# Kernel tuning notes

Hardware: AMD Instinct MI355X
Metric: run time of the kernel (lower is better)

## Reference

```python
import jax, jax.numpy as jnp
import numpy as np

L, D, H, KV, HD, KVL, I, PL = 8, 2048, 8, 2, 256, 4096, 8192, 256
FULL = (4,)          # layers with full (global) attention / global RoPE
POS = 2047           # current decode position (cache write slot)
N_REP = H // KV      # GQA expansion factor


def rms(x, eps=1e-6):
    # RMSNorm without scale (v_norm); scale applied by caller where needed
    return x * jax.lax.rsqrt(jnp.mean(x * x, axis=-1, keepdims=True) + eps)


def rope(x, cos, sin):
    half = HD // 2
    rot = jnp.concatenate([-x[..., half:], x[..., :half]], axis=-1)
    return x * cos + rot * sin


def _rope_tables(theta):
    inv = 1.0 / (theta ** (np.arange(0, HD, 2, dtype=np.float32) / HD))
    ang = jnp.asarray(POS * inv, dtype=jnp.float32)
    return jnp.concatenate([jnp.cos(ang)] * 2), jnp.concatenate([jnp.sin(ang)] * 2)


def setup_inputs() -> dict:
    key = jax.random.key(0)
    ks = jax.random.split(key, 24)
    r = lambda k, s, sc=0.02: jax.random.normal(k, s, jnp.float32) * sc
    gains = lambda k, s: 1.0 + jax.random.normal(k, s, jnp.float32) * 0.02
    cos_s, sin_s = _rope_tables(10000.0)
    cos_f, sin_f = _rope_tables(1000000.0)
    um = jnp.zeros((1, 1, KVL, 1), jnp.float32).at[0, 0, POS, 0].set(1.0)
    mask = jnp.where(jnp.arange(KVL) <= POS, 0.0, -1e9).astype(jnp.float32)
    return {
        "hidden_states": r(ks[0], (1, 1, D), 1.0),
        "causal_mask": mask,
        "update_mask": um,
        "per_layer_combined": r(ks[1], (1, 1, L * PL), 1.0),
        "cos_s": cos_s, "sin_s": sin_s, "cos_f": cos_f, "sin_f": sin_f,
        "K_in": r(ks[2], (L, KV, KVL, HD)),
        "V_in": r(ks[3], (L, KV, KVL, HD)),
        "w_q": r(ks[4], (L, H * HD, D)),
        "w_k": r(ks[5], (L, KV * HD, D)),
        "w_v": r(ks[6], (L, KV * HD, D)),
        "w_o": r(ks[7], (L, D, H * HD)),
        "g_in_ln": gains(ks[8], (L, D)),
        "g_q_norm": gains(ks[9], (L, HD)),
        "g_k_norm": gains(ks[10], (L, HD)),
        "g_post_attn_ln": gains(ks[11], (L, D)),
        "g_pre_ff_ln": gains(ks[12], (L, D)),
        "g_post_ff_ln": gains(ks[13], (L, D)),
        "w_gate": r(ks[14], (L, I, D)),
        "w_up": r(ks[15], (L, I, D)),
        "w_down": r(ks[16], (L, D, I)),
        "w_plg": r(ks[17], (L, PL, D)),
        "w_plp": r(ks[18], (L, D, PL)),
        "g_post_pl_ln": gains(ks[19], (L, D)),
        "layer_scalar": jnp.ones((L,), jnp.float32),
    }


def reference(hidden_states, causal_mask, update_mask, per_layer_combined,
              cos_s, sin_s, cos_f, sin_f, K_in, V_in,
              w_q, w_k, w_v, w_o,
              g_in_ln, g_q_norm, g_k_norm, g_post_attn_ln, g_pre_ff_ln, g_post_ff_ln,
              w_gate, w_up, w_down, w_plg, w_plp, g_post_pl_ln, layer_scalar):
    um = update_mask[0, 0]          # [KVL,1] one-hot at write position
    h = hidden_states[0, 0]         # [D], batch=1/seq=1 decode
    K_outs, V_outs = [], []
    for i in range(L):
        cos, sin = (cos_f, sin_f) if i in FULL else (cos_s, sin_s)
        # --- attention block ---
        res = h
        x = rms(h) * g_in_ln[i]
        q = rms((w_q[i] @ x).reshape(H, HD)) * g_q_norm[i]
        q = rope(q, cos, sin)                                   # [H,HD]
        k = rms((w_k[i] @ x).reshape(KV, HD)) * g_k_norm[i]
        k = rope(k, cos, sin)                                   # [KV,HD]
        v = rms((w_v[i] @ x).reshape(KV, HD))                    # v_norm (no scale)
        # full-tensor masked blend = KV cache write (faithful to source)
        Ko = K_in[i] * (1.0 - um) + k[:, None, :] * um          # [KV,KVL,HD]
        Vo = V_in[i] * (1.0 - um) + v[:, None, :] * um
        K_outs.append(Ko); V_outs.append(Vo)
        Ke = jnp.repeat(Ko, N_REP, axis=0)                      # GQA expand [H,KVL,HD]
        Ve = jnp.repeat(Vo, N_REP, axis=0)
        scores = jnp.einsum('hd,hkd->hk', q, Ke) + causal_mask  # no 1/sqrt(hd) in source
        attn = jax.nn.softmax(scores, axis=-1)
        ao = jnp.einsum('hk,hkd->hd', attn, Ve).reshape(H * HD)
        ao = rms(w_o[i] @ ao) * g_post_attn_ln[i]
        h = res + ao
        # --- gated MLP ---
        res = h
        xm = rms(h) * g_pre_ff_ln[i]
        m = w_down[i] @ (jax.nn.gelu(w_gate[i] @ xm, approximate=True) * (w_up[i] @ xm))
        h = res + rms(m) * g_post_ff_ln[i]
        # --- per-layer input gating ---
        res = h
        pls = per_layer_combined[0, 0, i * PL:(i + 1) * PL]     # [PL]
        g = jax.nn.gelu(w_plg[i] @ h, approximate=True) * pls
        h = res + rms(w_plp[i] @ g) * g_post_pl_ln[i]
        h = h * layer_scalar[i]
    return (h[None, None, :], jnp.stack(K_outs), jnp.stack(V_outs))
```

## Files before the change

kernel.cpp:

```cpp
#include <hip/hip_runtime.h>

#define NL   8
#define DIM  2048
#define NH   8
#define NKV  2
#define HD   256
#define KVL  4096
#define FFI  8192
#define PLD  256
#define POS  2047
#define NCH  128
#define CP   16

typedef float vfloat4 __attribute__((ext_vector_type(4)));

__device__ __forceinline__ float dot4(float4 a, float4 b){
  return a.x*b.x + a.y*b.y + a.z*b.z + a.w*b.w;
}

__device__ __forceinline__ float4 ntld4(const float4* p){
  vfloat4 v = __builtin_nontemporal_load((const vfloat4*)p);
  float4 r; r.x=v.x; r.y=v.y; r.z=v.z; r.w=v.w; return r;
}
__device__ __forceinline__ void ntst4(float4* p, float4 v){
  vfloat4 t; t.x=v.x; t.y=v.y; t.z=v.z; t.w=v.w;
  __builtin_nontemporal_store(t, (vfloat4*)p);
}

__device__ __forceinline__ float waveAllSum(float v){
#pragma unroll
  for(int o=1;o<64;o<<=1) v += __shfl_xor(v,o,64);
  return v;
}

__device__ __forceinline__ float blockSum256(float v, float* red){
  int lane = threadIdx.x & 63, w = threadIdx.x >> 6;
  v = waveAllSum(v);
  __syncthreads();
  if(lane==0) red[w] = v;
  __syncthreads();
  return red[0]+red[1]+red[2]+red[3];
}

__device__ __forceinline__ float gelu_tanh(float v){
  return 0.5f*v*(1.0f + tanhf(0.7978845608028654f*(v + 0.044715f*v*v*v)));
}

__device__ __forceinline__ float4 normRope(const float* __restrict__ raw, int lane,
    const float* __restrict__ gain, const float* __restrict__ cosT,
    const float* __restrict__ sinT, bool doRope){
  float4 v4 = ((const float4*)raw)[lane];
  float ss = waveAllSum(dot4(v4,v4));
  float sc = rsqrtf(ss*(1.f/HD) + 1e-6f);
  float4 n;
  if(gain){
    float4 g4 = ((const float4*)gain)[lane];
    n.x=v4.x*sc*g4.x; n.y=v4.y*sc*g4.y; n.z=v4.z*sc*g4.z; n.w=v4.w*sc*g4.w;
  } else {
    n.x=v4.x*sc; n.y=v4.y*sc; n.z=v4.z*sc; n.w=v4.w*sc;
  }
  if(!doRope) return n;
  float4 np;
  np.x=__shfl_xor(n.x,32,64); np.y=__shfl_xor(n.y,32,64);
  np.z=__shfl_xor(n.z,32,64); np.w=__shfl_xor(n.w,32,64);
  float4 c4 = ((const float4*)cosT)[lane];
  float4 s4 = ((const float4*)sinT)[lane];
  float sg = (lane < 32) ? -1.f : 1.f;
  float4 o;
  o.x = n.x*c4.x + sg*np.x*s4.x;
  o.y = n.y*c4.y + sg*np.y*s4.y;
  o.z = n.z*c4.z + sg*np.z*s4.z;
  o.w = n.w*c4.w + sg*np.w*s4.w;
  return o;
}

__global__ __launch_bounds__(256) void qkv_k(
    const float* __restrict__ Wq, const float* __restrict__ Wk,
    const float* __restrict__ Wv,
    const float* __restrict__ hFF, const float* __restrict__ u,
    const float* __restrict__ g_pl, const float* __restrict__ lsc,
    const float* __restrict__ g_in, const float* __restrict__ hidden,
    float* __restrict__ hRes, float* __restrict__ qkv){
  __shared__ float xs[DIM];
  __shared__ float red[4];
  int tid = threadIdx.x;
  float hv[8];
  if(hidden){
#pragma unroll
    for(int i=0;i<8;i++) hv[i] = hidden[tid + i*256];
  } else {
    float uv[8]; float ss1 = 0.f;
#pragma unroll
    for(int i=0;i<8;i++){ uv[i] = u[tid + i*256]; ss1 += uv[i]*uv[i]; }
    ss1 = blockSum256(ss1, red);
    float r1 = rsqrtf(ss1*(1.f/DIM) + 1e-6f);
    float ls = lsc[0];
#pragma unroll
    for(int i=0;i<8;i++){
      int idx = tid + i*256;
      hv[i] = (hFF[idx] + uv[i]*r1*g_pl[idx])*ls;
    }
  }
  float ss2 = 0.f;
#pragma unroll
  for(int i=0;i<8;i++) ss2 += hv[i]*hv[i];
  ss2 = blockSum256(ss2, red);
  float r2 = rsqrtf(ss2*(1.f/DIM) + 1e-6f);
#pragma unroll
  for(int i=0;i<8;i++){
    int idx = tid + i*256;
    xs[idx] = hv[i]*r2*g_in[idx];
    if(blockIdx.x==0) hRes[idx] = hv[i];
  }
  __syncthreads();
  int lane = tid & 63, wv = tid >> 6;
  int r = blockIdx.x*4 + wv;
  const float* W; int row;
  if(r < 2048){ W = Wq; row = r; }
  else if(r < 2560){ W = Wk; row = r - 2048; }
  else { W = Wv; row = r - 2560; }
  const float4* Wr = (const float4*)(W + (size_t)row*DIM);
  const float4* xs4 = (const float4*)xs;
  float4 w8[8];
#pragma unroll
  for(int i=0;i<8;i++) w8[i] = Wr[i*64+lane];
  float acc = 0.f;
#pragma unroll
  for(int i=0;i<8;i++) acc += dot4(w8[i], xs4[i*64+lane]);
  acc = waveAllSum(acc);
  if(lane==0) qkv[r] = acc;
}

__global__ __launch_bounds__(256) void attn_k(
    const float* __restrict__ qkvb,
    const float* __restrict__ gq, const float* __restrict__ gk,
    const float* __restrict__ cosT, const float* __restrict__ sinT,
    const float* __restrict__ Ki, const float* __restrict__ Vi,
    float* __restrict__ Kl, float* __restrict__ Vl,
    float* __restrict__ pm, float* __restrict__ pl, float* __restrict__ po){
  int b = blockIdx.x, tid = threadIdx.x, lane = tid & 63, wv = tid >> 6;

  if(b == NKV*NCH){
    int kvv = wv >> 1, isV = wv & 1;
    const float* raw = qkvb + (isV ? 2560 : 2048) + kvv*HD;
    float4 o = normRope(raw, lane, isV ? nullptr : gk, cosT, sinT, !isV);
    float* dst = (isV ? Vl : Kl) + ((size_t)kvv*KVL + POS)*HD;
    ((float4*)dst)[lane] = o;
    return;
  }
  if(b > NKV*NCH){
    int b2 = b - (NKV*NCH+1);
#pragma unroll
    for(int i=0;i<8;i++){
      int ri = b2*32 + wv*8 + i;
      int combo = ri >> 11;
      int pos = 2048 + (ri & 2047);
      size_t off = ((size_t)(combo&1)*KVL + pos)*HD;
      const float4* s = (const float4*)(((combo>>1) ? Vi : Ki) + off);
      float4* d = (float4*)(((combo>>1) ? Vl : Kl) + off);
      ntst4(d + lane, ntld4(s + lane));
    }
    return;
  }

  int kv = b & 1, c = b >> 1;
  __shared__ float q_s[4][HD];
  __shared__ float vf_s[HD];
  __shared__ float s_s[4][CP];
  __shared__ float s_w[4][CP];
  bool fresh = (c == NCH-1);

  { float4 o = normRope(qkvb + (kv*4 + wv)*HD, lane, gq, cosT, sinT, true);
    ((float4*)q_s[wv])[lane] = o; }
  float4 kf4 = {0,0,0,0};
  if(fresh){
    if(wv == 3) kf4 = normRope(qkvb + 2048 + kv*HD, lane, gk, cosT, sinT, true);
    if(wv == 1){
      float4 o = normRope(qkvb + 2560 + kv*HD, lane, nullptr, cosT, sinT, false);
      ((float4*)vf_s)[lane] = o;
    }
  }
  __syncthreads();

  float4 q4[4];
#pragma unroll
  for(int hh=0;hh<4;hh++) q4[hh] = ((const float4*)q_s[hh])[lane];
  const float4* Kp = (const float4*)(Ki + ((size_t)kv*KVL + c*CP)*HD);
  float4* Kd = (float4*)(Kl + ((size_t)kv*KVL + c*CP)*HD);
#pragma unroll
  for(int j=0;j<4;j++){
    int p = wv*4 + j;
    bool isFreshRow = (fresh && p==CP-1);
    float4 k4;
    if(isFreshRow) k4 = kf4;
    else {
      k4 = Kp[(size_t)p*64 + lane];
      ntst4(Kd + (size_t)p*64 + lane, k4);
    }
    float d0 = dot4(k4,q4[0]), d1 = dot4(k4,q4[1]);
    float d2 = dot4(k4,q4[2]), d3 = dot4(k4,q4[3]);
    d0 = waveAllSum(d0); d1 = waveAllSum(d1);
    d2 = waveAllSum(d2); d3 = waveAllSum(d3);
    if(lane==0){ s_s[0][p]=d0; s_s[1][p]=d1; s_s[2][p]=d2; s_s[3][p]=d3; }
  }
  __syncthreads();

  if(tid < 64){
    int hh = tid >> 4, pp = tid & 15;
    float s = s_s[hh][pp];
    float m = s;
#pragma unroll
    for(int o=1;o<16;o<<=1) m = fmaxf(m, __shfl_xor(m,o,64));
    float e = __expf(s - m);
    float ls = e;
#pragma unroll
    for(int o=1;o<16;o<<=1) ls += __shfl_xor(ls,o,64);
    s_w[hh][pp] = e;
    if(pp==0){ int hg = kv*4 + hh; pm[hg*NCH + c] = m; pl[hg*NCH + c] = ls; }
  }
  __syncthreads();

  int d = tid;
  const float* Vp = Vi + ((size_t)kv*KVL + c*CP)*HD;
  float* Vd = Vl + ((size_t)kv*KVL + c*CP)*HD;
  float vv[CP];
#pragma unroll
  for(int p2=0;p2<CP;p2++){
    bool isFreshRow = (fresh && p2==CP-1);
    if(isFreshRow) vv[p2] = vf_s[d];
    else {
      vv[p2] = Vp[(size_t)p2*HD + d];
      Vd[(size_t)p2*HD + d] = vv[p2];
    }
  }
  float acc[4] = {0.f,0.f,0.f,0.f};
#pragma unroll
  for(int p2=0;p2<CP;p2++){
#pragma unroll
    for(int hh=0;hh<4;hh++) acc[hh] += s_w[hh][p2]*vv[p2];
  }
#pragma unroll
  for(int hh=0;hh<4;hh++)
    po[((size_t)(kv*4+hh)*NCH + c)*HD + d] = acc[hh];
}

__global__ __launch_bounds__(256) void attn_c(const float* __restrict__ pm,
    const float* __restrict__ pl, const float* __restrict__ po, float* __restrict__ ao){
  int h = blockIdx.x, tid = threadIdx.x;
  __shared__ float sm[NCH], sl[NCH], se[NCH];
  if(tid < NCH){ sm[tid] = pm[h*NCH+tid]; sl[tid] = pl[h*NCH+tid]; }
  __syncthreads();
  float M = -1e30f;
  for(int c=0;c<NCH;c++) M = fmaxf(M, sm[c]);
  if(tid < NCH) se[tid] = __expf(sm[tid]-M);
  __syncthreads();
  float Lh = 0.f;
  for(int c=0;c<NCH;c++) Lh += sl[c]*se[c];
  float a0=0.f, a1=0.f, a2=0.f, a3=0.f;
#pragma unroll 1
  for(int c=0;c<NCH;c+=4){
    a0 += po[((size_t)h*NCH + c  )*HD + tid]*se[c];
    a1 += po[((size_t)h*NCH + c+1)*HD + tid]*se[c+1];
    a2 += po[((size_t)h*NCH + c+2)*HD + tid]*se[c+2];
    a3 += po[((size_t)h*NCH + c+3)*HD + tid]*se[c+3];
  }
  ao[h*HD + tid] = (a0+a1+a2+a3) / Lh;
}

template<int C>
__global__ __launch_bounds__(256) void gemv_k(const float* __restrict__ W,
    const float* __restrict__ x, float* __restrict__ y){
  __shared__ float xs[C];
  for(int i=threadIdx.x; i<C/4; i+=256)
    ((float4*)xs)[i] = ((const float4*)x)[i];
  __syncthreads();
  int lane = threadIdx.x & 63, wv = threadIdx.x >> 6;
  int r = blockIdx.x*4 + wv;
  const float4* Wr = (const float4*)(W + (size_t)r*C);
  const float4* xs4 = (const float4*)xs;
  float acc = 0.f;
#pragma unroll
  for(int ii=0;ii<C/2048;ii++){
    float4 w8[8];
#pragma unroll
    for(int i=0;i<8 && ii*8+i < C/256;i++) w8[i] = Wr[(ii*8+i)*64+lane];
#pragma unroll
    for(int i=0;i<8 && ii*8+i < C/256;i++) acc += dot4(w8[i], xs4[(ii*8+i)*64+lane]);
  }
  if(C < 2048){
    float4 w1 = Wr[lane];
    acc = dot4(w1, xs4[lane]);
  }
  acc = waveAllSum(acc);
  if(lane==0) y[r] = acc;
}

__global__ __launch_bounds__(256) void gateup_k(const float* __restrict__ Wg,
    const float* __restrict__ Wu, const float* __restrict__ y,
    const float* __restrict__ hRes, const float* __restrict__ g_pa,
    const float* __restrict__ g_pf, float* __restrict__ hMid, float* __restrict__ t){
  __shared__ float xs[DIM];
  __shared__ float red[4];
  int tid = threadIdx.x;
  float yv[8]; float ss1 = 0.f;
#pragma unroll
  for(int i=0;i<8;i++){ yv[i] = y[tid + i*256]; ss1 += yv[i]*yv[i]; }
  ss1 = blockSum256(ss1, red);
  float r1 = rsqrtf(ss1*(1.f/DIM) + 1e-6f);
  float hv[8]; float ss2 = 0.f;
#pragma unroll
  for(int i=0;i<8;i++){
    int idx = tid + i*256;
    hv[i] = hRes[idx] + yv[i]*r1*g_pa[idx];
    ss2 += hv[i]*hv[i];
  }
  ss2 = blockSum256(ss2, red);
  float r2 = rsqrtf(ss2*(1.f/DIM) + 1e-6f);
#pragma unroll
  for(int i=0;i<8;i++){
    int idx = tid + i*256;
    xs[idx] = hv[i]*r2*g_pf[idx];
    if(blockIdx.x==0) hMid[idx] = hv[i];
  }
  __syncthreads();
  int lane = tid & 63, wv = tid >> 6;
  int j = blockIdx.x*4 + wv;
  const float4* Gr = (const float4*)(Wg + (size_t)j*DIM);
  const float4* Ur = (const float4*)(Wu + (size_t)j*DIM);
  const float4* xs4 = (const float4*)xs;
  float4 g8[8], u8[8];
#pragma unroll
  for(int i=0;i<8;i++) g8[i] = Gr[i*64+lane];
#pragma unroll
  for(int i=0;i<8;i++) u8[i] = Ur[i*64+lane];
  float ag = 0.f, au = 0.f;
#pragma unroll
  for(int i=0;i<8;i++){
    float4 bv = xs4[i*64+lane];
    ag += dot4(g8[i], bv);
    au += dot4(u8[i], bv);
  }
  ag = waveAllSum(ag);
  au = waveAllSum(au);
  if(lane==0) t[j] = gelu_tanh(ag)*au;
}

__global__ __launch_bounds__(256) void down_k(const float* __restrict__ Wd,
    const float* __restrict__ t, float* __restrict__ mv){
  __shared__ float red[4];
  int tid = threadIdx.x, lane = tid & 63, wv = tid >> 6;
  int r = blockIdx.x;
  const float4* Wr = (const float4*)(Wd + (size_t)r*FFI) + wv*512;
  const float4* tp = (const float4*)t + wv*512;
  float4 w8[8], t8[8];
#pragma unroll
  for(int i=0;i<8;i++) w8[i] = Wr[i*64+lane];
#pragma unroll
  for(int i=0;i<8;i++) t8[i] = tp[i*64+lane];
  float acc = 0.f;
#pragma unroll
  for(int i=0;i<8;i++) acc += dot4(w8[i], t8[i]);
  acc = waveAllSum(acc);
  if(lane==0) red[wv] = acc;
  __syncthreads();
  if(tid==0) mv[r] = red[0]+red[1]+red[2]+red[3];
}

__global__ __launch_bounds__(256) void plg_k(const float* __restrict__ W,
    const float* __restrict__ mv, const float* __restrict__ hMid,
    const float* __restrict__ g_ff, const float* __restrict__ pls,
    float* __restrict__ hFFout, float* __restrict__ gb){
  __shared__ float xs[DIM];
  __shared__ float red[4];
  int tid = threadIdx.x;
  float mvv[8]; float ss1 = 0.f;
#pragma unroll
  for(int i=0;i<8;i++){ mvv[i] = mv[tid + i*256]; ss1 += mvv[i]*mvv[i]; }
  ss1 = blockSum256(ss1, red);
  float r1 = rsqrtf(ss1*(1.f/DIM) + 1e-6f);
#pragma unroll
  for(int i=0;i<8;i++){
    int idx = tid + i*256;
    float hc = hMid[idx] + mvv[i]*r1*g_ff[idx];
    xs[idx] = hc;
    if(blockIdx.x==0) hFFout[idx] = hc;
  }
  __syncthreads();
  int lane = tid & 63, wv = tid >> 6;
  int r = blockIdx.x*4 + wv;
  const float4* Wr = (const float4*)(W + (size_t)r*DIM);
  const float4* xs4 = (const float4*)xs;
  float4 w8[8];
#pragma unroll
  for(int i=0;i<8;i++) w8[i] = Wr[i*64+lane];
  float acc = 0.f;
#pragma unroll
  for(int i=0;i<8;i++) acc += dot4(w8[i], xs4[i*64+lane]);
  acc = waveAllSum(acc);
  if(lane==0) gb[r] = gelu_tanh(acc)*pls[r];
}

__global__ __launch_bounds__(256) void final_k(const float* __restrict__ u,
    const float* __restrict__ hFF, const float* __restrict__ g_pl,
    const float* __restrict__ lsc, float* __restrict__ out){
  __shared__ float red[4];
  int tid = threadIdx.x;
  float uv[8]; float ss1 = 0.f;
#pragma unroll
  for(int i=0;i<8;i++){ uv[i] = u[tid + i*256]; ss1 += uv[i]*uv[i]; }
  ss1 = blockSum256(ss1, red);
  float r1 = rsqrtf(ss1*(1.f/DIM) + 1e-6f);
  float ls = lsc[0];
#pragma unroll
  for(int i=0;i<8;i++){
    int idx = tid + i*256;
    out[idx] = (hFF[idx] + uv[i]*r1*g_pl[idx])*ls;
  }
}

extern "C" void kernel_launch(void* const* d_in, const int* in_sizes, int n_in,
                              void* d_out, int out_size, void* d_ws, size_t ws_size,
                              hipStream_t stream){
  const float* hidden   = (const float*)d_in[0];
  const float* plc      = (const float*)d_in[3];
  const float* cos_s    = (const float*)d_in[4];
  const float* sin_s    = (const float*)d_in[5];
  const float* cos_f    = (const float*)d_in[6];
  const float* sin_f    = (const float*)d_in[7];
  const float* K_in     = (const float*)d_in[8];
  const float* V_in     = (const float*)d_in[9];
  const float* w_q      = (const float*)d_in[10];
  const float* w_k      = (const float*)d_in[11];
  const float* w_v      = (const float*)d_in[12];
  const float* w_o      = (const float*)d_in[13];
  const float* g_in_ln  = (const float*)d_in[14];
  const float* g_q_norm = (const float*)d_in[15];
  const float* g_k_norm = (const float*)d_in[16];
  const float* g_pa_ln  = (const float*)d_in[17];
  const float* g_pf_ln  = (const float*)d_in[18];
  const float* g_ff_ln  = (const float*)d_in[19];
  const float* w_gate   = (const float*)d_in[20];
  const float* w_up     = (const float*)d_in[21];
  const float* w_down   = (const float*)d_in[22];
  const float* w_plg    = (const float*)d_in[23];
  const float* w_plp    = (const float*)d_in[24];
  const float* g_pl_ln  = (const float*)d_in[25];
  const float* l_scal   = (const float*)d_in[26];

  float* out  = (float*)d_out;
  float* outK = out + DIM;
  float* outV = outK + (size_t)NL*NKV*KVL*HD;

  float* ws   = (float*)d_ws;
  float* hRes = ws;
  float* hMid = ws + 2048;
  float* hFF  = ws + 4096;
  float* qkvb = ws + 6144;
  float* y    = ws + 9216;
  float* t    = ws + 11264;
  float* mv   = ws + 19456;
  float* gb   = ws + 21504;
  float* u    = ws + 21760;
  float* pm   = ws + 23808;
  float* pl   = ws + 24832;
  float* po   = ws + 25856;
  float* ao   = ws + 288000;

  for(int l=0;l<NL;l++){
    const float* cosT = (l==4) ? cos_f : cos_s;
    const float* sinT = (l==4) ? sin_f : sin_s;
    float* Kl = outK + (size_t)l*NKV*KVL*HD;
    float* Vl = outV + (size_t)l*NKV*KVL*HD;
    const float* Ki = K_in + (size_t)l*NKV*KVL*HD;
    const float* Vi = V_in + (size_t)l*NKV*KVL*HD;

    qkv_k<<<768,256,0,stream>>>(
        w_q + (size_t)l*NH*HD*DIM, w_k + (size_t)l*NKV*HD*DIM,
        w_v + (size_t)l*NKV*HD*DIM,
        hFF, u,
        (l>0) ? g_pl_ln + (size_t)(l-1)*DIM : g_pl_ln,
        (l>0) ? l_scal + (l-1) : l_scal,
        g_in_ln + (size_t)l*DIM,
        (l==0) ? hidden : nullptr,
        hRes, qkvb);

    attn_k<<<NKV*NCH+1+256,256,0,stream>>>(qkvb, g_q_norm + l*HD,
                                           g_k_norm + l*HD, cosT, sinT,
                                           Ki, Vi, Kl, Vl, pm, pl, po);

    attn_c<<<NH,256,0,stream>>>(pm, pl, po, ao);

    gemv_k<DIM><<<512,256,0,stream>>>(w_o + (size_t)l*DIM*NH*HD, ao, y);

    gateup_k<<<FFI/4,256,0,stream>>>(w_gate + (size_t)l*FFI*DIM,
                                     w_up + (size_t)l*FFI*DIM,
                                     y, hRes, g_pa_ln + (size_t)l*DIM,
                                     g_pf_ln + (size_t)l*DIM, hMid, t);

    down_k<<<DIM,256,0,stream>>>(w_down + (size_t)l*DIM*FFI, t, mv);

    plg_k<<<PLD/4,256,0,stream>>>(w_plg + (size_t)l*PLD*DIM, mv, hMid,
                                  g_ff_ln + (size_t)l*DIM, plc + l*PLD, hFF, gb);

    gemv_k<PLD><<<512,256,0,stream>>>(w_plp + (size_t)l*DIM*PLD, gb, u);
  }

  final_k<<<1,256,0,stream>>>(u, hFF, g_pl_ln + (size_t)(NL-1)*DIM,
                              l_scal + (NL-1), out);
}
```

Before: 787.8 us.

## Fuse dependent attention and FFN-tail stages into single kernels via atomic counters

Merges attention, attention-combine and o-projection into one launch, and down-proj, per-layer gate, per-layer projection and final norm into another. Later-stage blocks spin on global atomic counters until producer blocks signal completion. The goal is to cut kernel launch gaps and tail bubbles between the many small dependent stages. It depends on producer blocks being scheduled before consumers, which is not guaranteed and could deadlock, and it adds a memset plus spin-wait overhead.

```diff
diff --git a/kernel.cpp b/kernel.cpp
--- a/kernel.cpp
+++ b/kernel.cpp
@@ -74,6 +74,22 @@
   return o;
 }
 
+__device__ __forceinline__ void prodSignal(unsigned* c){
+  __syncthreads();
+  if(threadIdx.x == 0){
+    __builtin_amdgcn_fence(__ATOMIC_RELEASE, "agent");
+    __hip_atomic_fetch_add(c, 1u, __ATOMIC_RELAXED, __HIP_MEMORY_SCOPE_AGENT);
+  }
+}
+__device__ __forceinline__ void consWait(unsigned* c, unsigned n){
+  if(threadIdx.x == 0){
+    while(__hip_atomic_load(c, __ATOMIC_RELAXED, __HIP_MEMORY_SCOPE_AGENT) < n)
+      __builtin_amdgcn_s_sleep(2);
+    __builtin_amdgcn_fence(__ATOMIC_ACQUIRE, "agent");
+  }
+  __syncthreads();
+}
+
 __global__ __launch_bounds__(256) void qkv_k(
     const float* __restrict__ Wq, const float* __restrict__ Wk,
     const float* __restrict__ Wv,
@@ -131,25 +147,105 @@
   if(lane==0) qkv[r] = acc;
 }
 
-__global__ __launch_bounds__(256) void attn_k(
+__global__ __launch_bounds__(256,5) void attnfull_k(
     const float* __restrict__ qkvb,
     const float* __restrict__ gq, const float* __restrict__ gk,
     const float* __restrict__ cosT, const float* __restrict__ sinT,
     const float* __restrict__ Ki, const float* __restrict__ Vi,
     float* __restrict__ Kl, float* __restrict__ Vl,
-    float* __restrict__ pm, float* __restrict__ pl, float* __restrict__ po){
+    float* __restrict__ pm, float* __restrict__ pl, float* __restrict__ po,
+    const float* __restrict__ Wo, float* __restrict__ ao, float* __restrict__ y,
+    unsigned* cnt){
+  __shared__ float sh[2048];
   int b = blockIdx.x, tid = threadIdx.x, lane = tid & 63, wv = tid >> 6;
-
-  if(b == NKV*NCH){
+  unsigned* c_attn = cnt;
+  unsigned* c_comb = cnt + 16;
+
+  if(b < NKV*NCH){
+    int kv = b & 1, c = b >> 1;
+    float* q_s  = sh;
+    float* vf_s = sh + 1024;
+    float* s_sB = sh + 1280;
+    float* s_wB = sh + 1344;
+    bool fresh = (c == NCH-1);
+    { float4 o = normRope(qkvb + (kv*4 + wv)*HD, lane, gq, cosT, sinT, true);
+      ((float4*)(q_s + wv*HD))[lane] = o; }
+    float4 kf4 = {0,0,0,0};
+    if(fresh){
+      if(wv == 3) kf4 = normRope(qkvb + 2048 + kv*HD, lane, gk, cosT, sinT, true);
+      if(wv == 1){
+        float4 o = normRope(qkvb + 2560 + kv*HD, lane, nullptr, cosT, sinT, false);
+        ((float4*)vf_s)[lane] = o;
+      }
+    }
+    __syncthreads();
+    float4 q4[4];
+#pragma unroll
+    for(int hh=0;hh<4;hh++) q4[hh] = ((const float4*)(q_s + hh*HD))[lane];
+    const float4* Kp = (const float4*)(Ki + ((size_t)kv*KVL + c*CP)*HD);
+    float4* Kd = (float4*)(Kl + ((size_t)kv*KVL + c*CP)*HD);
+#pragma unroll
+    for(int j=0;j<4;j++){
+      int p = wv*4 + j;
+      bool isFreshRow = (fresh && p==CP-1);
+      float4 k4;
+      if(isFreshRow) k4 = kf4;
+      else {
+        k4 = Kp[(size_t)p*64 + lane];
+        ntst4(Kd + (size_t)p*64 + lane, k4);
+      }
+      float d0 = dot4(k4,q4[0]), d1 = dot4(k4,q4[1]);
+      float d2 = dot4(k4,q4[2]), d3 = dot4(k4,q4[3]);
+      d0 = waveAllSum(d0); d1 = waveAllSum(d1);
+      d2 = waveAllSum(d2); d3 = waveAllSum(d3);
+      if(lane==0){ s_sB[0*CP+p]=d0; s_sB[1*CP+p]=d1; s_sB[2*CP+p]=d2; s_sB[3*CP+p]=d3; }
+    }
+    __syncthreads();
+    if(tid < 64){
+      int hh = tid >> 4, pp = tid & 15;
+      float s = s_sB[hh*CP+pp];
+      float m = s;
+#pragma unroll
+      for(int o=1;o<16;o<<=1) m = fmaxf(m, __shfl_xor(m,o,64));
+      float e = __expf(s - m);
+      float ls = e;
+#pragma unroll
+      for(int o=1;o<16;o<<=1) ls += __shfl_xor(ls,o,64);
+      s_wB[hh*CP+pp] = e;
+      if(pp==0){ int hg = kv*4 + hh; pm[hg*NCH + c] = m; pl[hg*NCH + c] = ls; }
+    }
+    __syncthreads();
+    int d = tid;
+    const float* Vp = Vi + ((size_t)kv*KVL + c*CP)*HD;
+    float* Vd = Vl + ((size_t)kv*KVL + c*CP)*HD;
+    float vv[CP];
+#pragma unroll
+    for(int p2=0;p2<CP;p2++){
+      bool isFreshRow = (fresh && p2==CP-1);
+      if(isFreshRow) vv[p2] = vf_s[d];
+      else {
+        vv[p2] = Vp[(size_t)p2*HD + d];
+        Vd[(size_t)p2*HD + d] = vv[p2];
+      }
+    }
+    float acc[4] = {0.f,0.f,0.f,0.f};
+#pragma unroll
+    for(int p2=0;p2<CP;p2++){
+#pragma unroll
+      for(int hh=0;hh<4;hh++) acc[hh] += s_wB[hh*CP+p2]*vv[p2];
+    }
+#pragma unroll
+    for(int hh=0;hh<4;hh++)
+      po[((size_t)(kv*4+hh)*NCH + c)*HD + d] = acc[hh];
+    prodSignal(c_attn);
+  } else if(b == NKV*NCH){
     int kvv = wv >> 1, isV = wv & 1;
     const float* raw = qkvb + (isV ? 2560 : 2048) + kvv*HD;
     float4 o = normRope(raw, lane, isV ? nullptr : gk, cosT, sinT, !isV);
     float* dst = (isV ? Vl : Kl) + ((size_t)kvv*KVL + POS)*HD;
     ((float4*)dst)[lane] = o;
-    return;
-  }
-  if(b > NKV*NCH){
-    int b2 = b - (NKV*NCH+1);
+  } else if(b < 513){
+    int b2 = b - 257;
 #pragma unroll
     for(int i=0;i<8;i++){
       int ri = b2*32 + wv*8 + i;
@@ -160,139 +256,46 @@
       float4* d = (float4*)(((combo>>1) ? Vl : Kl) + off);
       ntst4(d + lane, ntld4(s + lane));
     }
-    return;
-  }
-
-  int kv = b & 1, c = b >> 1;
-  __shared__ float q_s[4][HD];
-  __shared__ float vf_s[HD];
-  __shared__ float s_s[4][CP];
-  __shared__ float s_w[4][CP];
-  bool fresh = (c == NCH-1);
-
-  { float4 o = normRope(qkvb + (kv*4 + wv)*HD, lane, gq, cosT, sinT, true);
-    ((float4*)q_s[wv])[lane] = o; }
-  float4 kf4 = {0,0,0,0};
-  if(fresh){
-    if(wv == 3) kf4 = normRope(qkvb + 2048 + kv*HD, lane, gk, cosT, sinT, true);
-    if(wv == 1){
-      float4 o = normRope(qkvb + 2560 + kv*HD, lane, nullptr, cosT, sinT, false);
-      ((float4*)vf_s)[lane] = o;
-    }
-  }
-  __syncthreads();
-
-  float4 q4[4];
-#pragma unroll
-  for(int hh=0;hh<4;hh++) q4[hh] = ((const float4*)q_s[hh])[lane];
-  const float4* Kp = (const float4*)(Ki + ((size_t)kv*KVL + c*CP)*HD);
-  float4* Kd = (float4*)(Kl + ((size_t)kv*KVL + c*CP)*HD);
-#pragma unroll
-  for(int j=0;j<4;j++){
-    int p = wv*4 + j;
-    bool isFreshRow = (fresh && p==CP-1);
-    float4 k4;
-    if(isFreshRow) k4 = kf4;
-    else {
-      k4 = Kp[(size_t)p*64 + lane];
-      ntst4(Kd + (size_t)p*64 + lane, k4);
-    }
-    float d0 = dot4(k4,q4[0]), d1 = dot4(k4,q4[1]);
-    float d2 = dot4(k4,q4[2]), d3 = dot4(k4,q4[3]);
-    d0 = waveAllSum(d0); d1 = waveAllSum(d1);
-    d2 = waveAllSum(d2); d3 = waveAllSum(d3);
-    if(lane==0){ s_s[0][p]=d0; s_s[1][p]=d1; s_s[2][p]=d2; s_s[3][p]=d3; }
-  }
-  __syncthreads();
-
-  if(tid < 64){
-    int hh = tid >> 4, pp = tid & 15;
-    float s = s_s[hh][pp];
-    float m = s;
-#pragma unroll
-    for(int o=1;o<16;o<<=1) m = fmaxf(m, __shfl_xor(m,o,64));
-    float e = __expf(s - m);
-    float ls = e;
-#pragma unroll
-    for(int o=1;o<16;o<<=1) ls += __shfl_xor(ls,o,64);
-    s_w[hh][pp] = e;
-    if(pp==0){ int hg = kv*4 + hh; pm[hg*NCH + c] = m; pl[hg*NCH + c] = ls; }
-  }
-  __syncthreads();
-
-  int d = tid;
-  const float* Vp = Vi + ((size_t)kv*KVL + c*CP)*HD;
-  float* Vd = Vl + ((size_t)kv*KVL + c*CP)*HD;
-  float vv[CP];
-#pragma unroll
-  for(int p2=0;p2<CP;p2++){
-    bool isFreshRow = (fresh && p2==CP-1);
-    if(isFreshRow) vv[p2] = vf_s[d];
-    else {
-      vv[p2] = Vp[(size_t)p2*HD + d];
-      Vd[(size_t)p2*HD + d] = vv[p2];
-    }
-  }
-  float acc[4] = {0.f,0.f,0.f,0.f};
-#pragma unroll
-  for(int p2=0;p2<CP;p2++){
-#pragma unroll
-    for(int hh=0;hh<4;hh++) acc[hh] += s_w[hh][p2]*vv[p2];
-  }
-#pragma unroll
-  for(int hh=0;hh<4;hh++)
-    po[((size_t)(kv*4+hh)*NCH + c)*HD + d] = acc[hh];
-}
-
-__global__ __launch_bounds__(256) void attn_c(const float* __restrict__ pm,
-    const float* __restrict__ pl, const float* __restrict__ po, float* __restrict__ ao){
-  int h = blockIdx.x, tid = threadIdx.x;
-  __shared__ float sm[NCH], sl[NCH], se[NCH];
-  if(tid < NCH){ sm[tid] = pm[h*NCH+tid]; sl[tid] = pl[h*NCH+tid]; }
-  __syncthreads();
-  float M = -1e30f;
-  for(int c=0;c<NCH;c++) M = fmaxf(M, sm[c]);
-  if(tid < NCH) se[tid] = __expf(sm[tid]-M);
-  __syncthreads();
-  float Lh = 0.f;
-  for(int c=0;c<NCH;c++) Lh += sl[c]*se[c];
-  float a0=0.f, a1=0.f, a2=0.f, a3=0.f;
+  } else if(b < 521){
+    consWait(c_attn, 256);
+    int h = b - 513;
+    float* sm = sh; float* sl = sh + 128; float* se = sh + 256;
+    if(tid < NCH){ sm[tid] = pm[h*NCH+tid]; sl[tid] = pl[h*NCH+tid]; }
+    __syncthreads();
+    float M = -1e30f;
+    for(int c=0;c<NCH;c++) M = fmaxf(M, sm[c]);
+    if(tid < NCH) se[tid] = __expf(sm[tid]-M);
+    __syncthreads();
+    float Lh = 0.f;
+    for(int c=0;c<NCH;c++) Lh += sl[c]*se[c];
+    float a0=0.f, a1=0.f, a2=0.f, a3=0.f;
 #pragma unroll 1
-  for(int c=0;c<NCH;c+=4){
-    a0 += po[((size_t)h*NCH + c  )*HD + tid]*se[c];
-    a1 += po[((size_t)h*NCH + c+1)*HD + tid]*se[c+1];
-    a2 += po[((size_t)h*NCH + c+2)*HD + tid]*se[c+2];
-    a3 += po[((size_t)h*NCH + c+3)*HD + tid]*se[c+3];
-  }
-  ao[h*HD + tid] = (a0+a1+a2+a3) / Lh;
-}
-
-template<int C>
-__global__ __launch_bounds__(256) void gemv_k(const float* __restrict__ W,
-    const float* __restrict__ x, float* __restrict__ y){
-  __shared__ float xs[C];
-  for(int i=threadIdx.x; i<C/4; i+=256)
-    ((float4*)xs)[i] = ((const float4*)x)[i];
-  __syncthreads();
-  int lane = threadIdx.x & 63, wv = threadIdx.x >> 6;
-  int r = blockIdx.x*4 + wv;
-  const float4* Wr = (const float4*)(W + (size_t)r*C);
-  const float4* xs4 = (const float4*)xs;
-  float acc = 0.f;
-#pragma unroll
-  for(int ii=0;ii<C/2048;ii++){
+    for(int c=0;c<NCH;c+=4){
+      a0 += po[((size_t)h*NCH + c  )*HD + tid]*se[c];
+      a1 += po[((size_t)h*NCH + c+1)*HD + tid]*se[c+1];
+      a2 += po[((size_t)h*NCH + c+2)*HD + tid]*se[c+2];
+      a3 += po[((size_t)h*NCH + c+3)*HD + tid]*se[c+3];
+    }
+    ao[h*HD + tid] = (a0+a1+a2+a3) / Lh;
+    prodSignal(c_comb);
+  } else {
+    consWait(c_comb, 8);
+    float4* sh4 = (float4*)sh;
+#pragma unroll
+    for(int i=0;i<2;i++) sh4[tid + i*256] = ((const float4*)ao)[tid + i*256];
+    __syncthreads();
+    int b2 = b - 521;
+    int r = b2*4 + wv;
+    const float4* Wr = (const float4*)(Wo + (size_t)r*DIM);
     float4 w8[8];
 #pragma unroll
-    for(int i=0;i<8 && ii*8+i < C/256;i++) w8[i] = Wr[(ii*8+i)*64+lane];
-#pragma unroll
-    for(int i=0;i<8 && ii*8+i < C/256;i++) acc += dot4(w8[i], xs4[(ii*8+i)*64+lane]);
-  }
-  if(C < 2048){
-    float4 w1 = Wr[lane];
-    acc = dot4(w1, xs4[lane]);
-  }
-  acc = waveAllSum(acc);
-  if(lane==0) y[r] = acc;
+    for(int i=0;i<8;i++) w8[i] = Wr[i*64+lane];
+    float acc = 0.f;
+#pragma unroll
+    for(int i=0;i<8;i++) acc += dot4(w8[i], sh4[i*64+lane]);
+    acc = waveAllSum(acc);
+    if(lane==0) y[r] = acc;
+  }
 }
 
 __global__ __launch_bounds__(256) void gateup_k(const float* __restrict__ Wg,
@@ -345,76 +348,101 @@
   if(lane==0) t[j] = gelu_tanh(ag)*au;
 }
 
-__global__ __launch_bounds__(256) void down_k(const float* __restrict__ Wd,
-    const float* __restrict__ t, float* __restrict__ mv){
-  __shared__ float red[4];
-  int tid = threadIdx.x, lane = tid & 63, wv = tid >> 6;
-  int r = blockIdx.x;
-  const float4* Wr = (const float4*)(Wd + (size_t)r*FFI) + wv*512;
-  const float4* tp = (const float4*)t + wv*512;
-  float4 w8[8], t8[8];
-#pragma unroll
-  for(int i=0;i<8;i++) w8[i] = Wr[i*64+lane];
-#pragma unroll
-  for(int i=0;i<8;i++) t8[i] = tp[i*64+lane];
-  float acc = 0.f;
-#pragma unroll
-  for(int i=0;i<8;i++) acc += dot4(w8[i], t8[i]);
-  acc = waveAllSum(acc);
-  if(lane==0) red[wv] = acc;
-  __syncthreads();
-  if(tid==0) mv[r] = red[0]+red[1]+red[2]+red[3];
-}
-
-__global__ __launch_bounds__(256) void plg_k(const float* __restrict__ W,
-    const float* __restrict__ mv, const float* __restrict__ hMid,
-    const float* __restrict__ g_ff, const float* __restrict__ pls,
-    float* __restrict__ hFFout, float* __restrict__ gb){
-  __shared__ float xs[DIM];
-  __shared__ float red[4];
-  int tid = threadIdx.x;
-  float mvv[8]; float ss1 = 0.f;
-#pragma unroll
-  for(int i=0;i<8;i++){ mvv[i] = mv[tid + i*256]; ss1 += mvv[i]*mvv[i]; }
-  ss1 = blockSum256(ss1, red);
-  float r1 = rsqrtf(ss1*(1.f/DIM) + 1e-6f);
-#pragma unroll
-  for(int i=0;i<8;i++){
-    int idx = tid + i*256;
-    float hc = hMid[idx] + mvv[i]*r1*g_ff[idx];
-    xs[idx] = hc;
-    if(blockIdx.x==0) hFFout[idx] = hc;
-  }
-  __syncthreads();
-  int lane = tid & 63, wv = tid >> 6;
-  int r = blockIdx.x*4 + wv;
-  const float4* Wr = (const float4*)(W + (size_t)r*DIM);
-  const float4* xs4 = (const float4*)xs;
-  float4 w8[8];
-#pragma unroll
-  for(int i=0;i<8;i++) w8[i] = Wr[i*64+lane];
-  float acc = 0.f;
-#pragma unroll
-  for(int i=0;i<8;i++) acc += dot4(w8[i], xs4[i*64+lane]);
-  acc = waveAllSum(acc);
-  if(lane==0) gb[r] = gelu_tanh(acc)*pls[r];
-}
-
-__global__ __launch_bounds__(256) void final_k(const float* __restrict__ u,
-    const float* __restrict__ hFF, const float* __restrict__ g_pl,
-    const float* __restrict__ lsc, float* __restrict__ out){
-  __shared__ float red[4];
-  int tid = threadIdx.x;
-  float uv[8]; float ss1 = 0.f;
-#pragma unroll
-  for(int i=0;i<8;i++){ uv[i] = u[tid + i*256]; ss1 += uv[i]*uv[i]; }
-  ss1 = blockSum256(ss1, red);
-  float r1 = rsqrtf(ss1*(1.f/DIM) + 1e-6f);
-  float ls = lsc[0];
-#pragma unroll
-  for(int i=0;i<8;i++){
-    int idx = tid + i*256;
-    out[idx] = (hFF[idx] + uv[i]*r1*g_pl[idx])*ls;
+__global__ __launch_bounds__(256,5) void downfull_k(
+    const float* __restrict__ Wd, const float* __restrict__ t,
+    float* __restrict__ mv,
+    const float* __restrict__ Wpg, const float* __restrict__ Wpp,
+    const float* __restrict__ hMid, const float* __restrict__ gff,
+    const float* __restrict__ pls, float* __restrict__ hFF,
+    float* __restrict__ gb, float* __restrict__ u,
+    const float* __restrict__ gpl, const float* __restrict__ lsc,
+    float* __restrict__ outv,
+    unsigned* cnt){
+  __shared__ float sh[2056];
+  int b = blockIdx.x, tid = threadIdx.x, lane = tid & 63, wv = tid >> 6;
+  unsigned* c_down = cnt + 32;
+  unsigned* c_plg  = cnt + 48;
+  unsigned* c_plp  = cnt + 64;
+
+  if(b < 1024){
+    int r0 = b*2;
+    int r = r0 + (wv>>1), half = wv & 1;
+    const float4* Wr = (const float4*)(Wd + (size_t)r*FFI) + half*1024;
+    const float4* tp = (const float4*)t + half*1024;
+    float acc = 0.f;
+#pragma unroll
+    for(int bb=0;bb<2;bb++){
+      float4 w8[8], t8[8];
+#pragma unroll
+      for(int i=0;i<8;i++) w8[i] = Wr[bb*512 + i*64 + lane];
+#pragma unroll
+      for(int i=0;i<8;i++) t8[i] = tp[bb*512 + i*64 + lane];
+#pragma unroll
+      for(int i=0;i<8;i++) acc += dot4(w8[i], t8[i]);
+    }
+    acc = waveAllSum(acc);
+    if(lane==0) sh[wv] = acc;
+    __syncthreads();
+    if(tid==0)  mv[r0]   = sh[0]+sh[1];
+    if(tid==64) mv[r0+1] = sh[2]+sh[3];
+    prodSignal(c_down);
+  } else if(b < 1088){
+    consWait(c_down, 1024);
+    float* red = sh + 2048;
+    float mvv[8]; float ss1 = 0.f;
+#pragma unroll
+    for(int i=0;i<8;i++){ mvv[i] = mv[tid + i*256]; ss1 += mvv[i]*mvv[i]; }
+    ss1 = blockSum256(ss1, red);
+    float r1 = rsqrtf(ss1*(1.f/DIM) + 1e-6f);
+#pragma unroll
+    for(int i=0;i<8;i++){
+      int idx = tid + i*256;
+      float hc = hMid[idx] + mvv[i]*r1*gff[idx];
+      sh[idx] = hc;
+      if(b==1024) hFF[idx] = hc;
+    }
+    __syncthreads();
+    int r = (b-1024)*4 + wv;
+    const float4* Wr = (const float4*)(Wpg + (size_t)r*DIM);
+    const float4* xs4 = (const float4*)sh;
+    float4 w8[8];
+#pragma unroll
+    for(int i=0;i<8;i++) w8[i] = Wr[i*64+lane];
+    float acc = 0.f;
+#pragma unroll
+    for(int i=0;i<8;i++) acc += dot4(w8[i], xs4[i*64+lane]);
+    acc = waveAllSum(acc);
+    if(lane==0) gb[r] = gelu_tanh(acc)*pls[r];
+    prodSignal(c_plg);
+  } else if(b < 1152){
+    consWait(c_plg, 64);
+    if(tid < 64) ((float4*)sh)[tid] = ((const float4*)gb)[tid];
+    __syncthreads();
+    const float4* gb4 = (const float4*)sh;
+#pragma unroll
+    for(int j=0;j<8;j++){
+      int r = (b-1088)*32 + wv*8 + j;
+      const float4* Wr = (const float4*)(Wpp + (size_t)r*PLD);
+      float acc = dot4(Wr[lane], gb4[lane]);
+      acc = waveAllSum(acc);
+      if(lane==0) u[r] = acc;
+    }
+    prodSignal(c_plp);
+  } else {
+    if(!outv) return;
+    consWait(c_plp, 64);
+    float* red = sh + 2048;
+    float uv[8]; float ss1 = 0.f;
+#pragma unroll
+    for(int i=0;i<8;i++){ uv[i] = u[tid + i*256]; ss1 += uv[i]*uv[i]; }
+    ss1 = blockSum256(ss1, red);
+    float r1 = rsqrtf(ss1*(1.f/DIM) + 1e-6f);
+    float ls = lsc[0];
+#pragma unroll
+    for(int i=0;i<8;i++){
+      int idx = tid + i*256;
+      outv[idx] = (hFF[idx] + uv[i]*r1*gpl[idx])*ls;
+    }
   }
 }
 
@@ -451,20 +479,24 @@
   float* outK = out + DIM;
   float* outV = outK + (size_t)NL*NKV*KVL*HD;
 
-  float* ws   = (float*)d_ws;
-  float* hRes = ws;
-  float* hMid = ws + 2048;
-  float* hFF  = ws + 4096;
-  float* qkvb = ws + 6144;
-  float* y    = ws + 9216;
-  float* t    = ws + 11264;
-  float* mv   = ws + 19456;
-  float* gb   = ws + 21504;
-  float* u    = ws + 21760;
-  float* pm   = ws + 23808;
-  float* pl   = ws + 24832;
-  float* po   = ws + 25856;
-  float* ao   = ws + 288000;
+  unsigned* cnt = (unsigned*)d_ws;
+
+  float* fws  = (float*)d_ws + 1024;
+  float* hRes = fws;
+  float* hMid = fws + 2048;
+  float* hFF  = fws + 4096;
+  float* qkvb = fws + 6144;
+  float* y    = fws + 9216;
+  float* t    = fws + 11264;
+  float* mv   = fws + 19456;
+  float* gb   = fws + 21504;
+  float* u    = fws + 21760;
+  float* pm   = fws + 23808;
+  float* pl   = fws + 24832;
+  float* po   = fws + 25856;
+  float* ao   = fws + 288000;
+
+  (void)hipMemsetAsync(d_ws, 0, 4096, stream);
 
   for(int l=0;l<NL;l++){
     const float* cosT = (l==4) ? cos_f : cos_s;
@@ -473,6 +505,7 @@
     float* Vl = outV + (size_t)l*NKV*KVL*HD;
     const float* Ki = K_in + (size_t)l*NKV*KVL*HD;
     const float* Vi = V_in + (size_t)l*NKV*KVL*HD;
+    unsigned* lc = cnt + l*80;
 
     qkv_k<<<768,256,0,stream>>>(
         w_q + (size_t)l*NH*HD*DIM, w_k + (size_t)l*NKV*HD*DIM,
@@ -484,27 +517,21 @@
         (l==0) ? hidden : nullptr,
         hRes, qkvb);
 
-    attn_k<<<NKV*NCH+1+256,256,0,stream>>>(qkvb, g_q_norm + l*HD,
-                                           g_k_norm + l*HD, cosT, sinT,
-                                           Ki, Vi, Kl, Vl, pm, pl, po);
-
-    attn_c<<<NH,256,0,stream>>>(pm, pl, po, ao);
-
-    gemv_k<DIM><<<512,256,0,stream>>>(w_o + (size_t)l*DIM*NH*HD, ao, y);
+    attnfull_k<<<1033,256,0,stream>>>(qkvb, g_q_norm + l*HD, g_k_norm + l*HD,
+                                      cosT, sinT, Ki, Vi, Kl, Vl,
+                                      pm, pl, po,
+                                      w_o + (size_t)l*DIM*NH*HD, ao, y, lc);
 
     gateup_k<<<FFI/4,256,0,stream>>>(w_gate + (size_t)l*FFI*DIM,
                                      w_up + (size_t)l*FFI*DIM,
                                      y, hRes, g_pa_ln + (size_t)l*DIM,
                                      g_pf_ln + (size_t)l*DIM, hMid, t);
 
-    down_k<<<DIM,256,0,stream>>>(w_down + (size_t)l*DIM*FFI, t, mv);
-
-    plg_k<<<PLD/4,256,0,stream>>>(w_plg + (size_t)l*PLD*DIM, mv, hMid,
-                                  g_ff_ln + (size_t)l*DIM, plc + l*PLD, hFF, gb);
-
-    gemv_k<PLD><<<512,256,0,stream>>>(w_plp + (size_t)l*DIM*PLD, gb, u);
-  }
-
-  final_k<<<1,256,0,stream>>>(u, hFF, g_pl_ln + (size_t)(NL-1)*DIM,
-                              l_scal + (NL-1), out);
-}
+    downfull_k<<<1153,256,0,stream>>>(
+        w_down + (size_t)l*DIM*FFI, t, mv,
+        w_plg + (size_t)l*PLD*DIM, w_plp + (size_t)l*DIM*PLD,
+        hMid, g_ff_ln + (size_t)l*DIM, plc + l*PLD, hFF, gb, u,
+        g_pl_ln + (size_t)l*DIM, l_scal + l,
+        (l==NL-1) ? out : nullptr, lc);
+  }
+}
```

Result: slower. 1.585 ms (+101.2%).
